# Kernel optimization log

Measured on AMD Instinct MI355X. Metric: run time of the kernel, lower is better.

Reference implementation:

```python
import jax, jax.numpy as jnp
import numpy as np

BATCH, HORIZON, NU, NY, K = 524288, 50, 4, 4, 32


def setup_inputs() -> dict:
    key = jax.random.key(0)
    ks = jax.random.split(key, 4)
    u = jax.random.normal(ks[0], (BATCH, HORIZON, NU), dtype=jnp.float32)
    y0 = jax.random.normal(ks[1], (BATCH, NY), dtype=jnp.float32)
    Wh = jax.random.normal(ks[2], (NU + NY, K), dtype=jnp.float32) * 0.3
    bh = jnp.zeros((K,), dtype=jnp.float32)
    Wo = jax.random.normal(ks[3], (K, 1), dtype=jnp.float32) * 0.3
    bo = jnp.zeros((1,), dtype=jnp.float32)
    return {"u": u, "y0": y0, "Wh": Wh, "bh": bh, "Wo": Wo, "bo": bo}


def reference(u, y0, Wh, bh, Wo, bo):
    u_t = jnp.transpose(u, (1, 0, 2))  # (T, B, NU) for scan

    def step(y_pred, ut):
        x = jnp.concatenate([ut, y_pred], axis=1)          # (B, NU+NY)
        h = jnp.tanh(x @ Wh + bh)                          # (B, K)
        pred = h @ Wo + bo                                 # (B, 1)
        # roll(shift=1)[:,1:] then prepend pred == drop last, prepend pred
        y_new = jnp.concatenate([pred, y_pred[:, :-1]], axis=1)
        return y_new, pred

    _, preds = jax.lax.scan(step, y0, u_t)  # preds: (T, B, 1)
    return jnp.transpose(preds, (1, 0, 2))  # (B, T, 1)
```

## Files before the change

kernel.cpp:

```cpp
#include <hip/hip_runtime.h>

#define T_HORIZON 50
#define NU 4
#define NY 4
#define KH 32
#define NW (8*KH + KH + KH + 1)
#define BPB 64

typedef float v2f __attribute__((ext_vector_type(2)));

__device__ __forceinline__ v2f fma2(v2f a, v2f b, v2f c) {
    return __builtin_elementwise_fma(a, b, c);
}

__device__ __forceinline__ float fast_tanh(float v) {
    float e = __builtin_amdgcn_exp2f(v * 2.88539008177792681472f);
    float r = __builtin_amdgcn_rcpf(e + 1.0f);
    return fmaf(-2.0f, r, 1.0f);
}

__global__ __launch_bounds__(256, 3) void rollout_kernel(
    const float* __restrict__ u,
    const float* __restrict__ y0g,
    const float* __restrict__ Whg,
    const float* __restrict__ bhg,
    const float* __restrict__ Wog,
    const float* __restrict__ bog,
    float* __restrict__ out)
{
    __shared__ float sW[NW];
    __shared__ __align__(16) float sOut[BPB * T_HORIZON];
    const int tid = threadIdx.x;

    if (tid < 8*KH) sW[tid] = Whg[tid];
    if (tid < 65) {
        float v;
        if (tid < KH)        v = bhg[tid];
        else if (tid < 2*KH) v = Wog[tid - KH];
        else                 v = bog[0];
        sW[8*KH + tid] = v;
    }
    __syncthreads();

    const int lane = tid & 63;
    const int widx = tid >> 6;
    const int bsub = lane & 15;
    const int jg   = lane >> 4;
    const int bl   = widx * 16 + bsub;
    const int b    = blockIdx.x * BPB + bl;

    v2f wh2[8][4];
#pragma unroll
    for (int i = 0; i < 8; ++i)
#pragma unroll
        for (int p = 0; p < 4; ++p)
            wh2[i][p] = v2f{sW[i*KH + jg + 8*p], sW[i*KH + jg + 8*p + 4]};
    v2f bh2[4];
    float work[8];
#pragma unroll
    for (int p = 0; p < 4; ++p)
        bh2[p] = v2f{sW[8*KH + jg + 8*p], sW[8*KH + jg + 8*p + 4]};
#pragma unroll
    for (int k = 0; k < 8; ++k)
        work[k] = sW[9*KH + jg + 4*k];
    const float bor = sW[10*KH];

    const float4* ub = (const float4*)(u + (size_t)b * T_HORIZON * NU);
    float4 yv = *(const float4*)(y0g + (size_t)b * NY);
    float y1 = yv.x, y2 = yv.y, y3 = yv.z, y4 = yv.w;

    float4 un = ub[0];
    for (int t = 0; t < T_HORIZON; ++t) {
        float4 uc = un;
        if (t + 1 < T_HORIZON) un = ub[t + 1];

        float aa[8];
#pragma unroll
        for (int p = 0; p < 4; ++p) {
            v2f a = fma2(v2f{uc.x, uc.x}, wh2[0][p], bh2[p]);
            a = fma2(v2f{uc.y, uc.y}, wh2[1][p], a);
            a = fma2(v2f{uc.z, uc.z}, wh2[2][p], a);
            a = fma2(v2f{uc.w, uc.w}, wh2[3][p], a);
            a = fma2(v2f{y1, y1},     wh2[4][p], a);
            a = fma2(v2f{y2, y2},     wh2[5][p], a);
            a = fma2(v2f{y3, y3},     wh2[6][p], a);
            a = fma2(v2f{y4, y4},     wh2[7][p], a);
            aa[2*p]     = a.x;
            aa[2*p + 1] = a.y;
        }

        float pcls = 0.0f;
#pragma unroll
        for (int k = 0; k < 8; ++k) {
            float m = fast_tanh(aa[k]) * work[k];
            pcls += m;
        }

        float partial = pcls;
        partial += __shfl_xor(partial, 16, 64);
        partial += __shfl_xor(partial, 32, 64);
        float pred = bor + partial;

        if (jg == 0) sOut[bl * T_HORIZON + t] = pred;

        y4 = y3; y3 = y2; y2 = y1; y1 = pred;
    }
    __syncthreads();

    const float4* s4 = (const float4*)sOut;
    float4* o4 = (float4*)(out + (size_t)blockIdx.x * BPB * T_HORIZON);
#pragma unroll
    for (int k = 0; k < 4; ++k) {
        int idx = k * 256 + tid;
        if (idx < (BPB * T_HORIZON) / 4) o4[idx] = s4[idx];
    }
}

extern "C" void kernel_launch(void* const* d_in, const int* in_sizes, int n_in,
                              void* d_out, int out_size, void* d_ws, size_t ws_size,
                              hipStream_t stream) {
    const float* u   = (const float*)d_in[0];
    const float* y0g = (const float*)d_in[1];
    const float* Whg = (const float*)d_in[2];
    const float* bhg = (const float*)d_in[3];
    const float* Wog = (const float*)d_in[4];
    const float* bog = (const float*)d_in[5];
    float* out = (float*)d_out;

    const int B = in_sizes[1] / NY;
    dim3 grid(B / BPB), block(256);
    rollout_kernel<<<grid, block, 0, stream>>>(u, y0g, Whg, bhg, Wog, bog, out);
}
```

Measured before the change: 326.6 us.

## Split hidden units across waves with LDS reduction and pre-staged wave-uniform weights

Reassigns work so each wave handles all 64 batch rows of a block for one quarter of the hidden units, making weight indices wave-uniform via readfirstlane. A small staging kernel writes weights in a permuted layout to the workspace so the main kernel can load them as scalar loads. The cross-lane shuffle reduction is replaced by a double-buffered LDS reduction with a block-wide barrier every time step. It also raises launch bounds occupancy to 6 and packs the tanh arithmetic into v2f ops. The risk is a __syncthreads per step serializing the waves, plus an extra kernel launch.

```diff
diff --git a/kernel.cpp b/kernel.cpp
--- a/kernel.cpp
+++ b/kernel.cpp
@@ -4,7 +4,6 @@
 #define NU 4
 #define NY 4
 #define KH 32
-#define NW (8*KH + KH + KH + 1)
 #define BPB 64
 
 typedef float v2f __attribute__((ext_vector_type(2)));
@@ -13,58 +12,61 @@
     return __builtin_elementwise_fma(a, b, c);
 }
 
-__device__ __forceinline__ float fast_tanh(float v) {
-    float e = __builtin_amdgcn_exp2f(v * 2.88539008177792681472f);
-    float r = __builtin_amdgcn_rcpf(e + 1.0f);
-    return fmaf(-2.0f, r, 1.0f);
+#define TANH_SCALE 2.88539008177792681472f
+
+__global__ void stage_weights(const float* __restrict__ Whg,
+                              const float* __restrict__ bhg,
+                              const float* __restrict__ Wog,
+                              float* __restrict__ ws) {
+    int idx = threadIdx.x;
+    if (idx < 320) {
+        int jg = idx / 80, r = idx % 80, i = r / 8, k = r % 8;
+        int j = jg + 4 * k;
+        float v = (i < 8) ? Whg[i * KH + j] : (i == 8 ? bhg[j] : Wog[j]);
+        ws[idx] = v;
+    }
 }
 
-__global__ __launch_bounds__(256, 3) void rollout_kernel(
+__global__ __launch_bounds__(256, 6) void rollout_kernel(
     const float* __restrict__ u,
     const float* __restrict__ y0g,
-    const float* __restrict__ Whg,
-    const float* __restrict__ bhg,
-    const float* __restrict__ Wog,
     const float* __restrict__ bog,
+    const float* __restrict__ wsW,
     float* __restrict__ out)
 {
-    __shared__ float sW[NW];
     __shared__ __align__(16) float sOut[BPB * T_HORIZON];
-    const int tid = threadIdx.x;
+    __shared__ float sRed[2][4][BPB];
 
-    if (tid < 8*KH) sW[tid] = Whg[tid];
-    if (tid < 65) {
-        float v;
-        if (tid < KH)        v = bhg[tid];
-        else if (tid < 2*KH) v = Wog[tid - KH];
-        else                 v = bog[0];
-        sW[8*KH + tid] = v;
-    }
-    __syncthreads();
+    const int tid  = threadIdx.x;
+    const int lane = tid & 63;
+    const int jg = __builtin_amdgcn_readfirstlane(tid >> 6);
 
-    const int lane = tid & 63;
-    const int widx = tid >> 6;
-    const int bsub = lane & 15;
-    const int jg   = lane >> 4;
-    const int bl   = widx * 16 + bsub;
-    const int b    = blockIdx.x * BPB + bl;
-
-    v2f wh2[8][4];
+    const float* wb = wsW + jg * 80;
+    v2f wh2[8][4], wor2[4];
 #pragma unroll
     for (int i = 0; i < 8; ++i)
 #pragma unroll
         for (int p = 0; p < 4; ++p)
-            wh2[i][p] = v2f{sW[i*KH + jg + 8*p], sW[i*KH + jg + 8*p + 4]};
-    v2f bh2[4];
-    float work[8];
+            wh2[i][p] = *(const v2f*)(wb + i * 8 + 2 * p);
 #pragma unroll
     for (int p = 0; p < 4; ++p)
-        bh2[p] = v2f{sW[8*KH + jg + 8*p], sW[8*KH + jg + 8*p + 4]};
+        wor2[p] = *(const v2f*)(wb + 9 * 8 + 2 * p);
+    const float bor = bog[0];
+
+    float bhs[8];
 #pragma unroll
-    for (int k = 0; k < 8; ++k)
-        work[k] = sW[9*KH + jg + 4*k];
-    const float bor = sW[10*KH];
+    for (int k = 0; k < 8; ++k) bhs[k] = wb[8 * 8 + k];
+#pragma unroll
+    for (int k = 0; k < 8; ++k) asm volatile("" : "+v"(bhs[k]));
+    v2f bh2[4];
+#pragma unroll
+    for (int p = 0; p < 4; ++p) bh2[p] = v2f{bhs[2 * p], bhs[2 * p + 1]};
 
+    const v2f scale2 = {TANH_SCALE, TANH_SCALE};
+    const v2f one2   = {1.0f, 1.0f};
+    const v2f ntwo2  = {-2.0f, -2.0f};
+
+    const int b = blockIdx.x * BPB + lane;
     const float4* ub = (const float4*)(u + (size_t)b * T_HORIZON * NU);
     float4 yv = *(const float4*)(y0g + (size_t)b * NY);
     float y1 = yv.x, y2 = yv.y, y3 = yv.z, y4 = yv.w;
@@ -74,34 +76,43 @@
         float4 uc = un;
         if (t + 1 < T_HORIZON) un = ub[t + 1];
 
-        float aa[8];
-#pragma unroll
-        for (int p = 0; p < 4; ++p) {
-            v2f a = fma2(v2f{uc.x, uc.x}, wh2[0][p], bh2[p]);
-            a = fma2(v2f{uc.y, uc.y}, wh2[1][p], a);
-            a = fma2(v2f{uc.z, uc.z}, wh2[2][p], a);
-            a = fma2(v2f{uc.w, uc.w}, wh2[3][p], a);
-            a = fma2(v2f{y1, y1},     wh2[4][p], a);
-            a = fma2(v2f{y2, y2},     wh2[5][p], a);
-            a = fma2(v2f{y3, y3},     wh2[6][p], a);
-            a = fma2(v2f{y4, y4},     wh2[7][p], a);
-            aa[2*p]     = a.x;
-            aa[2*p + 1] = a.y;
-        }
+        v2f ux = {uc.x, uc.x}, uy = {uc.y, uc.y}, uz = {uc.z, uc.z}, uw = {uc.w, uc.w};
+        v2f p1 = {y1, y1}, p2 = {y2, y2}, p3 = {y3, y3}, p4 = {y4, y4};
 
         float pcls = 0.0f;
 #pragma unroll
-        for (int k = 0; k < 8; ++k) {
-            float m = fast_tanh(aa[k]) * work[k];
-            pcls += m;
+        for (int p = 0; p < 4; ++p) {
+            v2f a = fma2(ux, wh2[0][p], bh2[p]);
+            a = fma2(uy, wh2[1][p], a);
+            a = fma2(uz, wh2[2][p], a);
+            a = fma2(uw, wh2[3][p], a);
+            a = fma2(p1, wh2[4][p], a);
+            a = fma2(p2, wh2[5][p], a);
+            a = fma2(p3, wh2[6][p], a);
+            a = fma2(p4, wh2[7][p], a);
+
+            v2f s = a * scale2;
+            float e0 = __builtin_amdgcn_exp2f(s.x);
+            float e1 = __builtin_amdgcn_exp2f(s.y);
+            v2f ep = v2f{e0, e1} + one2;
+            v2f r  = {__builtin_amdgcn_rcpf(ep.x), __builtin_amdgcn_rcpf(ep.y)};
+            v2f th = fma2(ntwo2, r, one2);
+            v2f m  = th * wor2[p];
+            pcls += m.x;
+            pcls += m.y;
         }
 
-        float partial = pcls;
-        partial += __shfl_xor(partial, 16, 64);
-        partial += __shfl_xor(partial, 32, 64);
+        const int buf = t & 1;
+        sRed[buf][jg][lane] = pcls;
+        __syncthreads();
+        float c0 = sRed[buf][0][lane];
+        float c1 = sRed[buf][1][lane];
+        float c2 = sRed[buf][2][lane];
+        float c3 = sRed[buf][3][lane];
+        float partial = (c0 + c1) + (c2 + c3);
         float pred = bor + partial;
 
-        if (jg == 0) sOut[bl * T_HORIZON + t] = pred;
+        if (jg == 0) sOut[lane * T_HORIZON + t] = pred;
 
         y4 = y3; y3 = y2; y2 = y1; y1 = pred;
     }
@@ -126,8 +137,11 @@
     const float* Wog = (const float*)d_in[4];
     const float* bog = (const float*)d_in[5];
     float* out = (float*)d_out;
+    float* ws  = (float*)d_ws;
+
+    stage_weights<<<1, 320, 0, stream>>>(Whg, bhg, Wog, ws);
 
     const int B = in_sizes[1] / NY;
     dim3 grid(B / BPB), block(256);
-    rollout_kernel<<<grid, block, 0, stream>>>(u, y0g, Whg, bhg, Wog, bog, out);
+    rollout_kernel<<<grid, block, 0, stream>>>(u, y0g, bog, ws, out);
 }
```

Measured after the change: 335.1 us. +2.6%, slower.
